# Optimization experiments

Measured on AMD Instinct MI355X. Metric: run time of the kernel, lower is better.

The kernel has to match this reference:

```python
import jax, jax.numpy as jnp
import numpy as np

W_PROFILE, W_PLANFORM, W_MEAN = 0.5, 0.3, 0.2
CELL_SIZE = 10.0
EPS = 1e-08


def _kernels():
    sobel_x = np.array([[-1, 0, 1], [-2, 0, 2], [-1, 0, 1]], np.float32) / 8.0
    sobel_y = np.array([[-1, -2, -1], [0, 0, 0], [1, 2, 1]], np.float32) / 8.0
    k_xx = np.array([[1, -2, 1], [1, -2, 1], [1, -2, 1]], np.float32) / 3.0
    k_yy = np.array([[1, 1, 1], [-2, -2, -2], [1, 1, 1]], np.float32) / 3.0
    k_xy = np.array([[-1, 0, 1], [0, 0, 0], [1, 0, -1]], np.float32) / 4.0
    # stack into one [5,1,3,3] OIHW kernel -> single fused conv for all 5 stencils
    return jnp.asarray(np.stack([sobel_x, sobel_y, k_xx, k_xy, k_yy])[:, None])

_K = _kernels()


def _curvatures(dem):
    # dem: [B,1,H,W] -> derivatives p,q,r,s,t each [B,1,H,W]
    d = jax.lax.conv_general_dilated(dem, _K, window_strides=(1, 1), padding='SAME',
                                     dimension_numbers=('NCHW', 'OIHW', 'NCHW'))
    p = d[:, 0:1] / CELL_SIZE
    q = d[:, 1:2] / CELL_SIZE
    r = d[:, 2:3] / CELL_SIZE ** 2
    s = d[:, 3:4] / CELL_SIZE ** 2
    t = d[:, 4:5] / CELL_SIZE ** 2
    p2, q2, pq = p * p, q * q, p * q
    denom1 = p2 + q2
    denom2 = (1 + denom1) ** 1.5
    profile = (r * p2 + 2 * s * pq + t * q2) / (denom1 * jnp.sqrt(1 + denom1) + EPS)
    planform = (r * q2 - 2 * s * pq + t * p2) / (denom1 ** 1.5 + EPS)
    mean = ((1 + q2) * r - 2 * pq * s + (1 + p2) * t) / (2 * denom2 + EPS)
    flat = denom1 < EPS
    profile = jnp.where(flat, 0.0, profile)
    planform = jnp.where(flat, 0.0, planform)
    return profile, planform, mean


def setup_inputs() -> dict:
    key = jax.random.key(0)
    k1, k2 = jax.random.split(key)
    shape = (16, 1, 1024, 1024)
    return {
        'pred': jax.random.normal(k1, shape, dtype=jnp.float32),
        'target': jax.random.normal(k2, shape, dtype=jnp.float32),
    }


def reference(pred, target):
    pp, pl, pm = _curvatures(pred)
    tp, tl, tm = _curvatures(target)
    loss_profile = jnp.mean(jnp.abs(pp - tp))
    loss_planform = jnp.mean(jnp.abs(pl - tl))
    loss_mean = jnp.mean(jnp.abs(pm - tm))
    return W_PROFILE * loss_profile + W_PLANFORM * loss_planform + W_MEAN * loss_mean
```

## Files before the change

### kernel.cpp

```cpp
#include <hip/hip_runtime.h>
#include <math.h>


constexpr int IMG_B = 16;
constexpr int IMG_H = 1024;
constexpr int IMG_W = 1024;
constexpr int ROWS  = 8;
constexpr int BLOCK = 256;
constexpr int TILES_Y = IMG_H / ROWS;
constexpr int NBLOCKS = IMG_B * TILES_Y;
constexpr float EPS = 1e-8f;

constexpr float A2  = 1.0f / 6400.0f;
constexpr float Bc  = 1.0f / 300.0f;
constexpr float C2  = 1.0f / 200.0f;

struct Row { float hx[4]; float hs[4]; float rs[4]; };

__device__ __forceinline__ void prep_row(const float* __restrict__ A, int y,
                                         bool okl, bool okr, Row& o)
{
    if ((unsigned)y < (unsigned)IMG_H) {
        const size_t off = (size_t)y << 10;
        const float4 v = *reinterpret_cast<const float4*>(A + off);
        const float l = okl ? A[off - 1] : 0.0f;
        const float r = okr ? A[off + 4] : 0.0f;
        const float w[6] = {l, v.x, v.y, v.z, v.w, r};
#pragma unroll
        for (int j = 0; j < 4; ++j) {
            const float e = w[j] + w[j + 2];
            o.hx[j] = w[j + 2] - w[j];
            o.hs[j] = fmaf(2.0f, w[j + 1], e);
            o.rs[j] = e + w[j + 1];
        }
    } else {
#pragma unroll
        for (int j = 0; j < 4; ++j) { o.hx[j] = 0.f; o.hs[j] = 0.f; o.rs[j] = 0.f; }
    }
}

__device__ __forceinline__ void curv(const Row& a, const Row& b, const Row& c, int j,
                                     float& prof, float& plan, float& mean)
{
    const float gx  = fmaf(2.0f, b.hx[j], a.hx[j] + c.hx[j]);
    const float gy  = c.hs[j] - a.hs[j];
    const float tot = (a.rs[j] + c.rs[j]) + b.rs[j];
    const float H   = (a.hs[j] + c.hs[j]) + b.hs[j];
    const float c1  = H - tot;
    const float rxx = fmaf(-3.0f, c1, tot);
    const float tyy = fmaf(-3.0f, b.rs[j], tot);
    const float sxy = a.hx[j] - c.hx[j];

    const float gx2 = gx * gx, gy2 = gy * gy, gxgy = gx * gy;
    const float g2  = gx2 + gy2;
    const float d1  = A2 * g2;
    const float od  = 1.0f + d1;

    const float sq_od = __builtin_amdgcn_sqrtf(od);
    const float sq_d1 = __builtin_amdgcn_sqrtf(d1);

    const float h1   = fmaf(tyy, gy2, rxx * gx2);
    const float h3   = fmaf(tyy, gx2, rxx * gy2);
    const float h2c  = C2 * (sxy * gxgy);
    const float nprof = A2 * fmaf(Bc, h1, h2c);
    const float nplan = A2 * fmaf(Bc, h3, -h2c);
    const float mnum  = fmaf(Bc, rxx + tyy, nplan);

    const float den_p = fmaf(d1, sq_od, EPS);
    const float den_l = fmaf(d1, sq_d1, EPS);
    const float den_m = fmaf(od + od, sq_od, EPS);

    prof = nprof * __builtin_amdgcn_rcpf(den_p);
    plan = nplan * __builtin_amdgcn_rcpf(den_l);
    mean = mnum  * __builtin_amdgcn_rcpf(den_m);
    if (d1 < EPS) { prof = 0.0f; plan = 0.0f; }
}

__global__ __launch_bounds__(BLOCK) void curv_loss_main(
    const float* __restrict__ pred, const float* __restrict__ targ,
    float* __restrict__ blocksums)
{
    const int tid = threadIdx.x;
    const int b   = blockIdx.x;
    const int img = b >> 7;
    const int ty  = b & (TILES_Y - 1);
    const int y0  = ty * ROWS;
    const size_t base = (size_t)img * (size_t)(IMG_H * IMG_W) + 4 * tid;
    const float* __restrict__ P = pred + base;
    const float* __restrict__ T = targ + base;
    const bool okl = (tid > 0);
    const bool okr = (tid < BLOCK - 1);

    Row pr[3], tr[3];
    prep_row(P, y0 - 1, okl, okr, pr[0]);
    prep_row(T, y0 - 1, okl, okr, tr[0]);
    prep_row(P, y0,     okl, okr, pr[1]);
    prep_row(T, y0,     okl, okr, tr[1]);

    float acc = 0.0f;
#pragma unroll
    for (int i = 0; i < ROWS; ++i) {
        const int ia = i % 3, ib = (i + 1) % 3, ic = (i + 2) % 3;
        prep_row(P, y0 + i + 1, okl, okr, pr[ic]);
        prep_row(T, y0 + i + 1, okl, okr, tr[ic]);
#pragma unroll
        for (int j = 0; j < 4; ++j) {
            float pp, pl, pm, qp, ql, qm;
            curv(pr[ia], pr[ib], pr[ic], j, pp, pl, pm);
            curv(tr[ia], tr[ib], tr[ic], j, qp, ql, qm);
            acc = fmaf(0.5f, fabsf(pp - qp), acc);
            acc = fmaf(0.3f, fabsf(pl - ql), acc);
            acc = fmaf(0.2f, fabsf(pm - qm), acc);
        }
    }

#pragma unroll
    for (int off = 32; off > 0; off >>= 1) acc += __shfl_down(acc, off, 64);
    __shared__ float ws[BLOCK / 64];
    const int lane = tid & 63, wid = tid >> 6;
    if (lane == 0) ws[wid] = acc;
    __syncthreads();
    if (tid == 0)
        blocksums[b] = (ws[0] + ws[1]) + (ws[2] + ws[3]);
}

__global__ __launch_bounds__(BLOCK) void curv_loss_final(
    const float* __restrict__ blocksums, float* __restrict__ out)
{
    const int tid = threadIdx.x;
    float v = 0.0f;
#pragma unroll
    for (int i = 0; i < NBLOCKS / BLOCK; ++i) v += blocksums[i * BLOCK + tid];
#pragma unroll
    for (int off = 32; off > 0; off >>= 1) v += __shfl_down(v, off, 64);
    __shared__ float ws[BLOCK / 64];
    const int lane = tid & 63, wid = tid >> 6;
    if (lane == 0) ws[wid] = v;
    __syncthreads();
    if (tid == 0) {
        const float tot = (ws[0] + ws[1]) + (ws[2] + ws[3]);
        out[0] = tot * (1.0f / (float)(IMG_B * IMG_H * IMG_W));
    }
}

extern "C" void kernel_launch(void* const* d_in, const int* in_sizes, int n_in,
                              void* d_out, int out_size, void* d_ws, size_t ws_size,
                              hipStream_t stream)
{
    const float* pred = (const float*)d_in[0];
    const float* targ = (const float*)d_in[1];
    float* out = (float*)d_out;
    float* blocksums = (float*)d_ws;

    curv_loss_main<<<NBLOCKS, BLOCK, 0, stream>>>(pred, targ, blocksums);
    curv_loss_final<<<1, BLOCK, 0, stream>>>(blocksums, out);
}
```

Before: 185.6 us.

## Split image width into two tiles with 2 columns per thread and cheaper curvature math

Each thread now handles 2 columns instead of 4 and the width is split across two blocks, doubling the grid. Each thread loads one unaligned 4-wide vector containing its halo, in place of a vector load plus two scalar neighbour loads. The curvature math is reworked: rsq replaces one sqrt, the profile and planform reciprocals share a single rcp, and the mean denominator becomes rsq cubed with the factor of 2 folded into the 0.1 weight. A launch-bounds occupancy hint of 6 is also added. The risks are a larger grid, more redundant halo traffic, and small numerical differences from the merged reciprocal.

```diff
diff --git a/kernel.cpp b/kernel.cpp
--- a/kernel.cpp
+++ b/kernel.cpp
@@ -7,47 +7,56 @@
 constexpr int IMG_W = 1024;
 constexpr int ROWS  = 8;
 constexpr int BLOCK = 256;
+constexpr int COLS_T = 2;
+constexpr int TILE_W = BLOCK * COLS_T;
+constexpr int TILES_X = IMG_W / TILE_W;
 constexpr int TILES_Y = IMG_H / ROWS;
-constexpr int NBLOCKS = IMG_B * TILES_Y;
+constexpr int NBLOCKS = IMG_B * TILES_Y * TILES_X;
 constexpr float EPS = 1e-8f;
 
-constexpr float A2  = 1.0f / 6400.0f;
-constexpr float Bc  = 1.0f / 300.0f;
-constexpr float C2  = 1.0f / 200.0f;
+constexpr float A2 = 1.0f / 6400.0f;
+constexpr float Bc = 1.0f / 300.0f;
+constexpr float C2 = 1.0f / 200.0f;
 
-struct Row { float hx[4]; float hs[4]; float rs[4]; };
+typedef float f4 __attribute__((ext_vector_type(4), aligned(4)));
 
-__device__ __forceinline__ void prep_row(const float* __restrict__ A, int y,
-                                         bool okl, bool okr, Row& o)
+struct Row { float hx[2], hs[2], rs[2]; };
+
+template<bool TILE0>
+__device__ __forceinline__ void prep_row(const float* __restrict__ Abase, int y,
+                                         bool edge, Row& o)
 {
     if ((unsigned)y < (unsigned)IMG_H) {
-        const size_t off = (size_t)y << 10;
-        const float4 v = *reinterpret_cast<const float4*>(A + off);
-        const float l = okl ? A[off - 1] : 0.0f;
-        const float r = okr ? A[off + 4] : 0.0f;
-        const float w[6] = {l, v.x, v.y, v.z, v.w, r};
-#pragma unroll
-        for (int j = 0; j < 4; ++j) {
-            const float e = w[j] + w[j + 2];
-            o.hx[j] = w[j + 2] - w[j];
-            o.hs[j] = fmaf(2.0f, w[j + 1], e);
-            o.rs[j] = e + w[j + 1];
+        const f4 L = *reinterpret_cast<const f4*>(Abase + ((size_t)y << 10));
+        float w0, w1, w2, w3;
+        if (TILE0) {
+            w0 = edge ? 0.0f : L.x;
+            w1 = edge ? L.x  : L.y;
+            w2 = edge ? L.y  : L.z;
+            w3 = edge ? L.z  : L.w;
+        } else {
+            w0 = edge ? L.y  : L.x;
+            w1 = edge ? L.z  : L.y;
+            w2 = edge ? L.w  : L.z;
+            w3 = edge ? 0.0f : L.w;
         }
+        const float e0 = w0 + w2, e1 = w1 + w3;
+        o.hx[0] = w2 - w0;              o.hx[1] = w3 - w1;
+        o.hs[0] = fmaf(2.0f, w1, e0);   o.hs[1] = fmaf(2.0f, w2, e1);
+        o.rs[0] = e0 + w1;              o.rs[1] = e1 + w2;
     } else {
-#pragma unroll
-        for (int j = 0; j < 4; ++j) { o.hx[j] = 0.f; o.hs[j] = 0.f; o.rs[j] = 0.f; }
+        o.hx[0] = o.hx[1] = o.hs[0] = o.hs[1] = o.rs[0] = o.rs[1] = 0.0f;
     }
 }
 
 __device__ __forceinline__ void curv(const Row& a, const Row& b, const Row& c, int j,
-                                     float& prof, float& plan, float& mean)
+                                     float& prof, float& plan, float& mean2)
 {
     const float gx  = fmaf(2.0f, b.hx[j], a.hx[j] + c.hx[j]);
     const float gy  = c.hs[j] - a.hs[j];
     const float tot = (a.rs[j] + c.rs[j]) + b.rs[j];
     const float H   = (a.hs[j] + c.hs[j]) + b.hs[j];
-    const float c1  = H - tot;
-    const float rxx = fmaf(-3.0f, c1, tot);
+    const float rxx = fmaf(-3.0f, H - tot, tot);
     const float tyy = fmaf(-3.0f, b.rs[j], tot);
     const float sxy = a.hx[j] - c.hx[j];
 
@@ -56,69 +65,87 @@
     const float d1  = A2 * g2;
     const float od  = 1.0f + d1;
 
-    const float sq_od = __builtin_amdgcn_sqrtf(od);
-    const float sq_d1 = __builtin_amdgcn_sqrtf(d1);
+    const float rsq_od = __builtin_amdgcn_rsqf(od);
+    const float sq_d1  = __builtin_amdgcn_sqrtf(d1);
+    const float sq_od  = od * rsq_od;
 
     const float h1   = fmaf(tyy, gy2, rxx * gx2);
     const float h3   = fmaf(tyy, gx2, rxx * gy2);
     const float h2c  = C2 * (sxy * gxgy);
-    const float nprof = A2 * fmaf(Bc, h1, h2c);
+    const float nprof = A2 * fmaf(Bc, h1,  h2c);
     const float nplan = A2 * fmaf(Bc, h3, -h2c);
     const float mnum  = fmaf(Bc, rxx + tyy, nplan);
 
     const float den_p = fmaf(d1, sq_od, EPS);
     const float den_l = fmaf(d1, sq_d1, EPS);
-    const float den_m = fmaf(od + od, sq_od, EPS);
+    const float rcpPL = __builtin_amdgcn_rcpf(den_p * den_l);
 
-    prof = nprof * __builtin_amdgcn_rcpf(den_p);
-    plan = nplan * __builtin_amdgcn_rcpf(den_l);
-    mean = mnum  * __builtin_amdgcn_rcpf(den_m);
+    prof  = (nprof * den_l) * rcpPL;
+    plan  = (nplan * den_p) * rcpPL;
+    mean2 = mnum * ((rsq_od * rsq_od) * rsq_od);
     if (d1 < EPS) { prof = 0.0f; plan = 0.0f; }
 }
 
-__global__ __launch_bounds__(BLOCK) void curv_loss_main(
+template<bool TILE0>
+__device__ __forceinline__ float run_tile(const float* __restrict__ P,
+                                          const float* __restrict__ T,
+                                          int y0, bool edge)
+{
+    Row pr[3], tr[3];
+    prep_row<TILE0>(P, y0 - 1, edge, pr[0]);
+    prep_row<TILE0>(T, y0 - 1, edge, tr[0]);
+    prep_row<TILE0>(P, y0,     edge, pr[1]);
+    prep_row<TILE0>(T, y0,     edge, tr[1]);
+
+    float acc = 0.0f;
+#pragma unroll
+    for (int i = 0; i < ROWS; ++i) {
+        const int ia = i % 3, ib = (i + 1) % 3, ic = (i + 2) % 3;
+        prep_row<TILE0>(P, y0 + i + 1, edge, pr[ic]);
+        prep_row<TILE0>(T, y0 + i + 1, edge, tr[ic]);
+#pragma unroll
+        for (int j = 0; j < 2; ++j) {
+            float pp, pl, pm, qp, ql, qm;
+            curv(pr[ia], pr[ib], pr[ic], j, pp, pl, pm);
+            curv(tr[ia], tr[ib], tr[ic], j, qp, ql, qm);
+            acc = fmaf(0.5f, fabsf(pp - qp), acc);
+            acc = fmaf(0.3f, fabsf(pl - ql), acc);
+            acc = fmaf(0.1f, fabsf(pm - qm), acc);
+        }
+    }
+    return acc;
+}
+
+__global__ __launch_bounds__(BLOCK, 6) void curv_loss_main(
     const float* __restrict__ pred, const float* __restrict__ targ,
     float* __restrict__ blocksums)
 {
     const int tid = threadIdx.x;
     const int b   = blockIdx.x;
-    const int img = b >> 7;
-    const int ty  = b & (TILES_Y - 1);
+    const int tx  = b & (TILES_X - 1);
+    const int ty  = (b >> 1) & (TILES_Y - 1);
+    const int img = b >> 8;
     const int y0  = ty * ROWS;
-    const size_t base = (size_t)img * (size_t)(IMG_H * IMG_W) + 4 * tid;
+    const int x0  = tx * TILE_W + COLS_T * tid;
+
+    int cload = x0 - 1;
+    bool edge;
+    if (tx == 0) { edge = (cload < 0);          if (edge) cload = 0; }
+    else         { edge = (cload > IMG_W - 4);  if (edge) cload = IMG_W - 4; }
+
+    const size_t base = (size_t)img * (size_t)(IMG_H * IMG_W) + cload;
     const float* __restrict__ P = pred + base;
     const float* __restrict__ T = targ + base;
-    const bool okl = (tid > 0);
-    const bool okr = (tid < BLOCK - 1);
 
-    Row pr[3], tr[3];
-    prep_row(P, y0 - 1, okl, okr, pr[0]);
-    prep_row(T, y0 - 1, okl, okr, tr[0]);
-    prep_row(P, y0,     okl, okr, pr[1]);
-    prep_row(T, y0,     okl, okr, tr[1]);
+    const float acc = (tx == 0) ? run_tile<true >(P, T, y0, edge)
+                                : run_tile<false>(P, T, y0, edge);
 
-    float acc = 0.0f;
+    float a = acc;
 #pragma unroll
-    for (int i = 0; i < ROWS; ++i) {
-        const int ia = i % 3, ib = (i + 1) % 3, ic = (i + 2) % 3;
-        prep_row(P, y0 + i + 1, okl, okr, pr[ic]);
-        prep_row(T, y0 + i + 1, okl, okr, tr[ic]);
-#pragma unroll
-        for (int j = 0; j < 4; ++j) {
-            float pp, pl, pm, qp, ql, qm;
-            curv(pr[ia], pr[ib], pr[ic], j, pp, pl, pm);
-            curv(tr[ia], tr[ib], tr[ic], j, qp, ql, qm);
-            acc = fmaf(0.5f, fabsf(pp - qp), acc);
-            acc = fmaf(0.3f, fabsf(pl - ql), acc);
-            acc = fmaf(0.2f, fabsf(pm - qm), acc);
-        }
-    }
-
-#pragma unroll
-    for (int off = 32; off > 0; off >>= 1) acc += __shfl_down(acc, off, 64);
+    for (int off = 32; off > 0; off >>= 1) a += __shfl_down(a, off, 64);
     __shared__ float ws[BLOCK / 64];
     const int lane = tid & 63, wid = tid >> 6;
-    if (lane == 0) ws[wid] = acc;
+    if (lane == 0) ws[wid] = a;
     __syncthreads();
     if (tid == 0)
         blocksums[b] = (ws[0] + ws[1]) + (ws[2] + ws[3]);
```

Result: slower. 246.5 us (+32.8%).
